# Performance work log

Measured on AMD Instinct MI355X. Metric: run time of the kernel, lower is better.

The kernel has to match this reference:

```python
import jax, jax.numpy as jnp
import numpy as np

EPS = 1e-6


def setup_inputs() -> dict:
    key = jax.random.key(0)
    k1, k2, k3, k4, k5, k6, k7 = jax.random.split(key, 7)
    b, n, p, h = 8, 4096, 16, 128
    hidden, rdim = 128, 64
    sq_features = jax.random.normal(k1, (b, p, h), dtype=jnp.float32)
    point_features = jax.random.normal(k2, (b, n, h), dtype=jnp.float32)
    assign_matrix = jax.random.uniform(k3, (b, n, p), dtype=jnp.float32)
    # MLP params: Linear(4h -> hidden), Linear(hidden -> rdim)
    s1 = 1.0 / np.sqrt(4 * h)
    s2 = 1.0 / np.sqrt(hidden)
    W1 = jax.random.uniform(k4, (4 * h, hidden), minval=-s1, maxval=s1, dtype=jnp.float32)
    b1 = jax.random.uniform(k5, (hidden,), minval=-s1, maxval=s1, dtype=jnp.float32)
    W2 = jax.random.uniform(k6, (hidden, rdim), minval=-s2, maxval=s2, dtype=jnp.float32)
    b2 = jax.random.uniform(k7, (rdim,), minval=-s2, maxval=s2, dtype=jnp.float32)
    return {"sq_features": sq_features, "point_features": point_features,
            "assign_matrix": assign_matrix, "W1": W1, "b1": b1, "W2": W2, "b2": b2}


def reference(sq_features, point_features, assign_matrix, W1, b1, W2, b2):
    # mass: (b, p) total assignment weight per primitive
    mass = jnp.maximum(assign_matrix.sum(axis=1), EPS)
    # weighted mean pooling: (b, p, h)
    pooled = jnp.einsum('bnp,bnh->bph', assign_matrix, point_features) / mass[..., None]
    # weighted per-point features, masked max over points: (b, n, p, h) -> (b, p, h)
    weighted = assign_matrix[..., None] * point_features[:, :, None, :]
    inactive = (assign_matrix <= EPS)[..., None]  # (b, n, p, 1)
    weighted = jnp.where(inactive, -jnp.inf, weighted)
    max_features = weighted.max(axis=1)
    max_features = jnp.where(jnp.isfinite(max_features), max_features,
                             jnp.zeros_like(max_features))
    # weighted variance about the pooled mean: (b, p, h)
    diff = point_features[:, :, None, :] - pooled[:, None, :, :]  # (b, n, p, h)
    var = (assign_matrix[..., None] * jnp.square(diff)).sum(axis=1) / mass[..., None]
    pooled_stats = jnp.concatenate([pooled, max_features, var], axis=-1)  # (b, p, 3h)
    residual_input = jnp.concatenate([sq_features, pooled_stats], axis=-1)  # (b, p, 4h)
    hdn = jax.nn.relu(residual_input @ W1 + b1)
    return hdn @ W2 + b2
```

## Files before the change

### kernel.cpp

```cpp
#include <hip/hip_runtime.h>
#include <math.h>

#define BB 8
#define NN 4096
#define PP 16
#define HH 128
#define SS 64
#define NS 64
#define HID 128
#define RD 64
#define EPSF 1e-6f

__global__ __launch_bounds__(512, 4) void k1_partials(
    const float* __restrict__ point,
    const float* __restrict__ assign,
    float* __restrict__ wsS1,
    float* __restrict__ wsS2,
    float* __restrict__ wsM,
    float* __restrict__ wsS0)
{
    __shared__ float lds_a[NS * PP];
    const int blk = blockIdx.x;
    const int b = blk >> 6;
    const int s = blk & (SS - 1);
    const int n0 = s * NS;
    const int tid = threadIdx.x;
    const int h = tid & (HH - 1);
    const int p0 = (tid >> 7) * 4;

    const float* aptr = assign + (size_t)b * NN * PP + (size_t)n0 * PP;
    lds_a[tid]       = aptr[tid];
    lds_a[tid + 512] = aptr[tid + 512];
    __syncthreads();

    float s1[4], s2[4], m[4];
    #pragma unroll
    for (int p = 0; p < 4; ++p) { s1[p] = 0.f; s2[p] = 0.f; m[p] = -INFINITY; }

    const float* xptr = point + (size_t)b * NN * HH + (size_t)n0 * HH + h;
    #pragma unroll 8
    for (int nn = 0; nn < NS; ++nn) {
        float x = xptr[(size_t)nn * HH];
        float4 av = *(const float4*)&lds_a[nn * PP + p0];
        float t;
        t = av.x * x; s1[0] += t; s2[0] = fmaf(t, x, s2[0]); m[0] = fmaxf(m[0], t);
        t = av.y * x; s1[1] += t; s2[1] = fmaf(t, x, s2[1]); m[1] = fmaxf(m[1], t);
        t = av.z * x; s1[2] += t; s2[2] = fmaf(t, x, s2[2]); m[2] = fmaxf(m[2], t);
        t = av.w * x; s1[3] += t; s2[3] = fmaf(t, x, s2[3]); m[3] = fmaxf(m[3], t);
    }

    const size_t base = (size_t)blk * PP * HH + h;
    #pragma unroll
    for (int p = 0; p < 4; ++p) {
        size_t idx = base + (size_t)(p0 + p) * HH;
        wsS1[idx] = s1[p];
        wsS2[idx] = s2[p];
        wsM[idx]  = m[p];
    }

    if (tid < PP) {
        float s0 = 0.f;
        #pragma unroll 16
        for (int nn = 0; nn < NS; ++nn) s0 += lds_a[nn * PP + tid];
        wsS0[(size_t)blk * PP + tid] = s0;
    }
}

__global__ __launch_bounds__(512) void k2_finish(
    const float* __restrict__ sq,
    const float* __restrict__ W1,
    const float* __restrict__ b1,
    const float* __restrict__ W2,
    const float* __restrict__ b2,
    const float* __restrict__ wsS1, const float* __restrict__ wsS2,
    const float* __restrict__ wsM,  const float* __restrict__ wsS0,
    float* __restrict__ out)
{
    __shared__ float lds1[16 * HH], lds2[16 * HH], ldsm[16 * HH];
    __shared__ float lds0[SS];
    __shared__ float r[4 * HH];
    __shared__ float part[4 * HID];
    __shared__ float h2[HID];
    __shared__ float part2[8 * RD];

    const int blk = blockIdx.x;
    const int b = blk >> 4;
    const int p = blk & (PP - 1);
    const int tid = threadIdx.x;
    const int h4 = (tid & 31) * 4;
    const int sub = tid >> 5;

    float4 a1 = make_float4(0.f, 0.f, 0.f, 0.f);
    float4 a2 = make_float4(0.f, 0.f, 0.f, 0.f);
    float4 am = make_float4(-INFINITY, -INFINITY, -INFINITY, -INFINITY);
    #pragma unroll
    for (int si = 0; si < SS / 16; ++si) {
        const int s = sub * (SS / 16) + si;
        const size_t idx = ((size_t)(b * SS + s) * PP + p) * HH + h4;
        float4 v1 = *(const float4*)&wsS1[idx];
        float4 v2 = *(const float4*)&wsS2[idx];
        float4 vm = *(const float4*)&wsM[idx];
        a1.x += v1.x; a1.y += v1.y; a1.z += v1.z; a1.w += v1.w;
        a2.x += v2.x; a2.y += v2.y; a2.z += v2.z; a2.w += v2.w;
        am.x = fmaxf(am.x, vm.x); am.y = fmaxf(am.y, vm.y);
        am.z = fmaxf(am.z, vm.z); am.w = fmaxf(am.w, vm.w);
    }
    *(float4*)&lds1[sub * HH + h4] = a1;
    *(float4*)&lds2[sub * HH + h4] = a2;
    *(float4*)&ldsm[sub * HH + h4] = am;
    if (tid < SS) lds0[tid] = wsS0[(size_t)(b * SS + tid) * PP + p];
    __syncthreads();

    if (tid < HH) {
        const int h = tid;
        float s1 = 0.f, s2 = 0.f, m = -INFINITY;
        #pragma unroll
        for (int k = 0; k < 16; ++k) {
            s1 += lds1[k * HH + h];
            s2 += lds2[k * HH + h];
            m = fmaxf(m, ldsm[k * HH + h]);
        }
        float s0 = 0.f;
        #pragma unroll
        for (int k = 0; k < SS; ++k) s0 += lds0[k];
        float mass = fmaxf(s0, EPSF);
        float pooled = s1 / mass;
        float var = (s2 - 2.f * pooled * s1 + pooled * pooled * s0) / mass;
        float maxf = (m == -INFINITY) ? 0.f : m;
        r[h]          = sq[(size_t)blk * HH + h];
        r[HH + h]     = pooled;
        r[2 * HH + h] = maxf;
        r[3 * HH + h] = var;
    }
    __syncthreads();

    {
        const int j = tid & (HID - 1);
        const int qt = tid >> 7;
        const int k0 = qt * 128;
        float acc = 0.f;
        #pragma unroll 8
        for (int k = 0; k < 128; ++k)
            acc = fmaf(r[k0 + k], W1[(size_t)(k0 + k) * HID + j], acc);
        part[qt * HID + j] = acc;
    }
    __syncthreads();
    if (tid < HID)
        h2[tid] = fmaxf(b1[tid] + part[tid] + part[HID + tid]
                        + part[2 * HID + tid] + part[3 * HID + tid], 0.f);
    __syncthreads();

    {
        const int o = tid & (RD - 1);
        const int g = tid >> 6;
        const int i0 = g * (HID / 8);
        float acc = 0.f;
        #pragma unroll
        for (int i = 0; i < HID / 8; ++i)
            acc = fmaf(h2[i0 + i], W2[(size_t)(i0 + i) * RD + o], acc);
        part2[g * RD + o] = acc;
    }
    __syncthreads();
    if (tid < RD) {
        float acc = b2[tid];
        #pragma unroll
        for (int g = 0; g < 8; ++g) acc += part2[g * RD + tid];
        out[(size_t)blk * RD + tid] = acc;
    }
}

extern "C" void kernel_launch(void* const* d_in, const int* in_sizes, int n_in,
                              void* d_out, int out_size, void* d_ws, size_t ws_size,
                              hipStream_t stream) {
    const float* sq     = (const float*)d_in[0];
    const float* point  = (const float*)d_in[1];
    const float* assign = (const float*)d_in[2];
    const float* W1     = (const float*)d_in[3];
    const float* b1     = (const float*)d_in[4];
    const float* W2     = (const float*)d_in[5];
    const float* b2     = (const float*)d_in[6];
    float* out = (float*)d_out;

    float* ws = (float*)d_ws;
    const size_t PH = (size_t)BB * SS * PP * HH;
    float* wsS1 = ws;
    float* wsS2 = ws + PH;
    float* wsM  = ws + 2 * PH;
    float* wsS0 = ws + 3 * PH;

    k1_partials<<<BB * SS, 512, 0, stream>>>(point, assign, wsS1, wsS2, wsM, wsS0);
    k2_finish<<<BB * PP, 512, 0, stream>>>(sq, W1, b1, W2, b2,
                                           wsS1, wsS2, wsM, wsS0, out);
}
```

Before: 92.47 us.

## Retile k1 partials to float4 h-vectors with in-block LDS tree reduction over n

Each thread now loads a float4 of point features and handles 4 h-columns times 4 primitives over a quarter of the 64-point slice. The four n-subgroups are then combined through a two-stage shared-memory tree reduction, and only one subgroup writes the partials with vector stores. The aim is wider global loads, more reuse of each loaded x across primitives, and fewer scalar stores. In exchange it needs 48KB of extra LDS and more registers, which may reduce occupancy under launch_bounds(512,4).

```diff
diff --git a/kernel.cpp b/kernel.cpp
--- a/kernel.cpp
+++ b/kernel.cpp
@@ -20,50 +20,105 @@
     float* __restrict__ wsS0)
 {
     __shared__ float lds_a[NS * PP];
+    __shared__ float cb[2][3][PP][HH];
     const int blk = blockIdx.x;
     const int b = blk >> 6;
     const int s = blk & (SS - 1);
     const int n0 = s * NS;
     const int tid = threadIdx.x;
-    const int h = tid & (HH - 1);
-    const int p0 = (tid >> 7) * 4;
+    const int h4 = (tid & 31) * 4;
+    const int p0 = ((tid >> 5) & 3) * 4;
+    const int nsub = tid >> 7;
 
     const float* aptr = assign + (size_t)b * NN * PP + (size_t)n0 * PP;
     lds_a[tid]       = aptr[tid];
     lds_a[tid + 512] = aptr[tid + 512];
     __syncthreads();
 
-    float s1[4], s2[4], m[4];
-    #pragma unroll
-    for (int p = 0; p < 4; ++p) { s1[p] = 0.f; s2[p] = 0.f; m[p] = -INFINITY; }
-
-    const float* xptr = point + (size_t)b * NN * HH + (size_t)n0 * HH + h;
-    #pragma unroll 8
-    for (int nn = 0; nn < NS; ++nn) {
-        float x = xptr[(size_t)nn * HH];
-        float4 av = *(const float4*)&lds_a[nn * PP + p0];
-        float t;
-        t = av.x * x; s1[0] += t; s2[0] = fmaf(t, x, s2[0]); m[0] = fmaxf(m[0], t);
-        t = av.y * x; s1[1] += t; s2[1] = fmaf(t, x, s2[1]); m[1] = fmaxf(m[1], t);
-        t = av.z * x; s1[2] += t; s2[2] = fmaf(t, x, s2[2]); m[2] = fmaxf(m[2], t);
-        t = av.w * x; s1[3] += t; s2[3] = fmaf(t, x, s2[3]); m[3] = fmaxf(m[3], t);
-    }
-
-    const size_t base = (size_t)blk * PP * HH + h;
+    float4 s1[4], s2[4], m4[4];
     #pragma unroll
     for (int p = 0; p < 4; ++p) {
-        size_t idx = base + (size_t)(p0 + p) * HH;
-        wsS1[idx] = s1[p];
-        wsS2[idx] = s2[p];
-        wsM[idx]  = m[p];
-    }
-
+        s1[p] = make_float4(0.f, 0.f, 0.f, 0.f);
+        s2[p] = make_float4(0.f, 0.f, 0.f, 0.f);
+        m4[p] = make_float4(-INFINITY, -INFINITY, -INFINITY, -INFINITY);
+    }
+
+    const float* xptr = point + (size_t)b * NN * HH + (size_t)(n0 + nsub * 16) * HH + h4;
+    #pragma unroll 2
+    for (int i = 0; i < 16; ++i) {
+        float4 x = *(const float4*)&xptr[(size_t)i * HH];
+        const int nn = nsub * 16 + i;
+        float4 av = *(const float4*)&lds_a[nn * PP + p0];
+        float xx0 = x.x * x.x, xx1 = x.y * x.y, xx2 = x.z * x.z, xx3 = x.w * x.w;
+        #pragma unroll
+        for (int p = 0; p < 4; ++p) {
+            float a = (p == 0) ? av.x : (p == 1) ? av.y : (p == 2) ? av.z : av.w;
+            float t0 = a * x.x, t1 = a * x.y, t2 = a * x.z, t3 = a * x.w;
+            s1[p].x += t0; s1[p].y += t1; s1[p].z += t2; s1[p].w += t3;
+            s2[p].x = fmaf(a, xx0, s2[p].x); s2[p].y = fmaf(a, xx1, s2[p].y);
+            s2[p].z = fmaf(a, xx2, s2[p].z); s2[p].w = fmaf(a, xx3, s2[p].w);
+            m4[p].x = fmaxf(m4[p].x, t0); m4[p].y = fmaxf(m4[p].y, t1);
+            m4[p].z = fmaxf(m4[p].z, t2); m4[p].w = fmaxf(m4[p].w, t3);
+        }
+    }
+
+    float s0 = 0.f;
     if (tid < PP) {
-        float s0 = 0.f;
         #pragma unroll 16
         for (int nn = 0; nn < NS; ++nn) s0 += lds_a[nn * PP + tid];
-        wsS0[(size_t)blk * PP + tid] = s0;
-    }
+    }
+
+    if (nsub >= 2) {
+        const int buf = nsub - 2;
+        #pragma unroll
+        for (int p = 0; p < 4; ++p) {
+            *(float4*)&cb[buf][0][p0 + p][h4] = s1[p];
+            *(float4*)&cb[buf][1][p0 + p][h4] = s2[p];
+            *(float4*)&cb[buf][2][p0 + p][h4] = m4[p];
+        }
+    }
+    __syncthreads();
+    if (nsub < 2) {
+        const int buf = nsub;
+        #pragma unroll
+        for (int p = 0; p < 4; ++p) {
+            float4 v1 = *(const float4*)&cb[buf][0][p0 + p][h4];
+            float4 v2 = *(const float4*)&cb[buf][1][p0 + p][h4];
+            float4 vm = *(const float4*)&cb[buf][2][p0 + p][h4];
+            s1[p].x += v1.x; s1[p].y += v1.y; s1[p].z += v1.z; s1[p].w += v1.w;
+            s2[p].x += v2.x; s2[p].y += v2.y; s2[p].z += v2.z; s2[p].w += v2.w;
+            m4[p].x = fmaxf(m4[p].x, vm.x); m4[p].y = fmaxf(m4[p].y, vm.y);
+            m4[p].z = fmaxf(m4[p].z, vm.z); m4[p].w = fmaxf(m4[p].w, vm.w);
+        }
+    }
+    __syncthreads();
+    if (nsub == 1) {
+        #pragma unroll
+        for (int p = 0; p < 4; ++p) {
+            *(float4*)&cb[0][0][p0 + p][h4] = s1[p];
+            *(float4*)&cb[0][1][p0 + p][h4] = s2[p];
+            *(float4*)&cb[0][2][p0 + p][h4] = m4[p];
+        }
+    }
+    __syncthreads();
+    if (nsub == 0) {
+        const size_t base = (size_t)blk * PP * HH + h4;
+        #pragma unroll
+        for (int p = 0; p < 4; ++p) {
+            float4 v1 = *(const float4*)&cb[0][0][p0 + p][h4];
+            float4 v2 = *(const float4*)&cb[0][1][p0 + p][h4];
+            float4 vm = *(const float4*)&cb[0][2][p0 + p][h4];
+            s1[p].x += v1.x; s1[p].y += v1.y; s1[p].z += v1.z; s1[p].w += v1.w;
+            s2[p].x += v2.x; s2[p].y += v2.y; s2[p].z += v2.z; s2[p].w += v2.w;
+            m4[p].x = fmaxf(m4[p].x, vm.x); m4[p].y = fmaxf(m4[p].y, vm.y);
+            m4[p].z = fmaxf(m4[p].z, vm.z); m4[p].w = fmaxf(m4[p].w, vm.w);
+            size_t idx = base + (size_t)(p0 + p) * HH;
+            *(float4*)&wsS1[idx] = s1[p];
+            *(float4*)&wsS2[idx] = s2[p];
+            *(float4*)&wsM[idx]  = m4[p];
+        }
+    }
+    if (tid < PP) wsS0[(size_t)blk * PP + tid] = s0;
 }
 
 __global__ __launch_bounds__(512) void k2_finish(
```

Result: slower. 94.97 us (+2.7%).
